# Performance work log

Hardware: AMD Instinct MI355X
Metric: run time of the kernel (lower is better)

The kernel has to match this reference:

```python
import jax, jax.numpy as jnp
import numpy as np

B, N, NPOINT, K = 16, 4096, 1024, 8
CIN, COUT = 128, 256
RADIUS = 0.2
BN_EPS = 1e-5


def fps(pts, npoint):
    # pts: [B, N, 3] -> indices [B, npoint], farthest point sampling starting at index 0
    b, n, _ = pts.shape

    def body(carry, _):
        dists, last = carry  # dists [B,N], last [B]
        cur = jnp.take_along_axis(pts, last[:, None, None], axis=1)  # [B,1,3]
        d = jnp.sum((pts - cur) ** 2, axis=-1)  # [B,N]
        dists = jnp.minimum(dists, d)
        nxt = jnp.argmax(dists, axis=-1).astype(jnp.int32)
        return (dists, nxt), last

    init = (jnp.full((b, n), jnp.finfo(pts.dtype).max, pts.dtype),
            jnp.zeros((b,), jnp.int32))
    _, idxs = jax.lax.scan(body, init, None, length=npoint)  # [npoint, B]
    return idxs.T  # [B, npoint]


def ball_query(new_xyz, pts, radius, k):
    # new_xyz [B,S,3], pts [B,N,3] -> idx [B,S,k] (pad with first in-ball index, pointnet2 semantics)
    n = pts.shape[1]
    d2 = jnp.sum((new_xyz[:, :, None, :] - pts[:, None, :, :]) ** 2, axis=-1)  # [B,S,N]
    cand = jnp.where(d2 <= radius * radius, jnp.arange(n, dtype=jnp.int32), n)
    idx = jnp.sort(cand, axis=-1)[..., :k]  # first k in-ball indices (center always in-ball)
    idx = jnp.where(idx == n, idx[..., :1], idx)
    return idx


def setup_inputs() -> dict:
    key = jax.random.key(0)
    ks = jax.random.split(key, 8)
    xyz = jax.random.uniform(ks[0], (B, 3, N), dtype=jnp.float32)
    feat = jax.random.normal(ks[1], (B, CIN, N), dtype=jnp.float32)
    conv_w = jax.random.normal(ks[2], (COUT, CIN), dtype=jnp.float32) * (1.0 / np.sqrt(CIN))
    conv_b = jax.random.normal(ks[3], (COUT,), dtype=jnp.float32) * 0.01
    bn_gamma = jax.random.uniform(ks[4], (COUT,), dtype=jnp.float32, minval=0.5, maxval=1.5)
    bn_beta = jax.random.normal(ks[5], (COUT,), dtype=jnp.float32) * 0.1
    bn_mean = jax.random.normal(ks[6], (COUT,), dtype=jnp.float32) * 0.1
    bn_var = jax.random.uniform(ks[7], (COUT,), dtype=jnp.float32, minval=0.5, maxval=1.5)
    return {"xyz": xyz, "feat": feat, "conv_w": conv_w, "conv_b": conv_b,
            "bn_gamma": bn_gamma, "bn_beta": bn_beta, "bn_mean": bn_mean, "bn_var": bn_var}


def reference(xyz, feat, conv_w, conv_b, bn_gamma, bn_beta, bn_mean, bn_var):
    pts = jnp.transpose(xyz, (0, 2, 1))   # [B,N,3]
    fts = jnp.transpose(feat, (0, 2, 1))  # [B,N,F]

    fps_idx = fps(pts, NPOINT)                                        # [B,S]
    new_xyz = jnp.take_along_axis(pts, fps_idx[..., None], axis=1)    # [B,S,3]

    idx = ball_query(new_xyz, pts, RADIUS, K)                          # [B,S,K]
    grouped = jax.vmap(lambda f, i: f[i])(fts, idx)                    # [B,S,K,F]

    # shared pointwise Conv1d (kernel 1) + BatchNorm (inference stats) + ReLU
    x = jnp.einsum('bskf,of->bsko', grouped, conv_w) + conv_b          # [B,S,K,COUT]
    x = bn_gamma * (x - bn_mean) / jnp.sqrt(bn_var + BN_EPS) + bn_beta
    x = jax.nn.relu(x)
    new_feat = jnp.max(x, axis=2)                                      # [B,S,COUT]
    return new_xyz, new_feat
```

## Files before the change

kernel.cpp:

```cpp
#include <hip/hip_runtime.h>
#include <hip/hip_bf16.h>
#include <stdint.h>

#define Bn   16
#define Nn   4096
#define Sn   1024
#define Kn   8
#define CINn 128
#define COUTn 256

static __device__ __forceinline__ float sqdist(float ax, float ay, float az,
                                               float bx, float by, float bz) {
    float dx = __fsub_rn(ax, bx);
    float dy = __fsub_rn(ay, by);
    float dz = __fsub_rn(az, bz);
    return __fadd_rn(__fadd_rn(__fmul_rn(dx, dx), __fmul_rn(dy, dy)), __fmul_rn(dz, dz));
}

static __device__ __forceinline__ unsigned long long u64max(unsigned long long a,
                                                            unsigned long long b) {
    return a > b ? a : b;
}

template <int CTRL>
static __device__ __forceinline__ void dpp_max_level(int& lo, int& hi) {
    int olo = __builtin_amdgcn_update_dpp(lo, lo, CTRL, 0xF, 0xF, false);
    int ohi = __builtin_amdgcn_update_dpp(hi, hi, CTRL, 0xF, 0xF, false);
    unsigned long long o = ((unsigned long long)(unsigned)ohi << 32) | (unsigned)olo;
    unsigned long long k = ((unsigned long long)(unsigned)hi << 32) | (unsigned)lo;
    if (o > k) { lo = olo; hi = ohi; }
}

static __device__ __forceinline__ unsigned long long wave_max_u64(unsigned long long key) {
    int lo = (int)(unsigned)(key & 0xFFFFFFFFull);
    int hi = (int)(unsigned)(key >> 32);
    dpp_max_level<0x111>(lo, hi);
    dpp_max_level<0x112>(lo, hi);
    dpp_max_level<0x114>(lo, hi);
    dpp_max_level<0x118>(lo, hi);
    dpp_max_level<0x142>(lo, hi);
    dpp_max_level<0x143>(lo, hi);
    unsigned flo = (unsigned)__builtin_amdgcn_readlane(lo, 63);
    unsigned fhi = (unsigned)__builtin_amdgcn_readlane(hi, 63);
    return ((unsigned long long)fhi << 32) | flo;
}

__global__ __launch_bounds__(256) void k_fps(const float* __restrict__ xyz,
                                             float* __restrict__ out_xyz) {
    __shared__ __align__(16) float xs[Nn], ys[Nn], zs[Nn];
    __shared__ __align__(16) unsigned long long gbuf[2][4];
    const int b = blockIdx.x;
    const int tid = threadIdx.x;
    const int wid = tid >> 6, lane = tid & 63;
    const float* base = xyz + (size_t)b * 3 * Nn;
    for (int i = tid; i < Nn; i += 256) {
        xs[i] = base[i];
        ys[i] = base[Nn + i];
        zs[i] = base[2 * Nn + i];
    }
    __syncthreads();
    float px[16], py[16], pz[16], dist[16];
#pragma unroll
    for (int j = 0; j < 16; ++j) {
        int p = tid + j * 256;
        px[j] = xs[p]; py[j] = ys[p]; pz[j] = zs[p];
        dist[j] = 3.402823466e+38f;
    }
    int last = 0;
    if (tid == 0) {
        out_xyz[(size_t)(b * Sn) * 3 + 0] = xs[0];
        out_xyz[(size_t)(b * Sn) * 3 + 1] = ys[0];
        out_xyz[(size_t)(b * Sn) * 3 + 2] = zs[0];
    }
    for (int s = 1; s < Sn; ++s) {
        const float cx = xs[last], cy = ys[last], cz = zs[last];
        float mv = -1.0f; int mi = 0;
#pragma unroll
        for (int j = 0; j < 16; ++j) {
            float d = sqdist(px[j], py[j], pz[j], cx, cy, cz);
            float nd = fminf(dist[j], d);
            dist[j] = nd;
            if (nd > mv) { mv = nd; mi = tid + j * 256; }
        }
        unsigned long long key =
            ((unsigned long long)__float_as_uint(mv) << 32) | (unsigned)(Nn - 1 - mi);
        key = wave_max_u64(key);
        if (lane == 0) gbuf[s & 1][wid] = key;
        __syncthreads();
        const ulonglong2 g0 = *(const ulonglong2*)&gbuf[s & 1][0];
        const ulonglong2 g1 = *(const ulonglong2*)&gbuf[s & 1][2];
        key = u64max(u64max(g0.x, g0.y), u64max(g1.x, g1.y));
        const int nl = Nn - 1 - (int)(unsigned)(key & 0xFFFFFFFFull);
        if (tid == 0) {
            out_xyz[(size_t)(b * Sn + s) * 3 + 0] = xs[nl];
            out_xyz[(size_t)(b * Sn + s) * 3 + 1] = ys[nl];
            out_xyz[(size_t)(b * Sn + s) * 3 + 2] = zs[nl];
        }
        last = nl;
    }
}

static __device__ __forceinline__ void wave_ball(const float* __restrict__ base,
                                                 float cx, float cy, float cz,
                                                 int lane, int* bslot) {
    int cnt = 0;
    int idx0 = -1;
    for (int chunk = 0; chunk < Nn / 64; ++chunk) {
        const int p = chunk * 64 + lane;
        const float d2 = sqdist(base[p], base[Nn + p], base[2 * Nn + p], cx, cy, cz);
        const bool in = (d2 <= 0.04f);
        const unsigned long long m = __ballot(in);
        if (m != 0ull) {
            if (idx0 < 0) idx0 = chunk * 64 + __builtin_ctzll(m);
            const int rank = cnt + __popcll(m & ((1ull << lane) - 1ull));
            if (in && rank < Kn)
                bslot[rank] = p;
            cnt += __popcll(m);
            if (cnt >= Kn) break;
        }
    }
    if (lane < Kn && lane >= cnt)
        bslot[lane] = idx0;
}

__global__ __launch_bounds__(512) void k_feat(const float* __restrict__ xyz,
                                              const float* __restrict__ out_xyz,
                                              const float* __restrict__ feat,
                                              const float* __restrict__ conv_w,
                                              const float* __restrict__ conv_b,
                                              const float* __restrict__ bn_g,
                                              const float* __restrict__ bn_b,
                                              const float* __restrict__ bn_m,
                                              const float* __restrict__ bn_v,
                                              float* __restrict__ out_feat) {
    __shared__ float Wc[32][COUTn + 1];
    __shared__ __align__(16) float At[8][Kn][36];
    __shared__ int bidx[8][Kn];
    const int tid = threadIdx.x;
    const int wave = tid >> 6, lane = tid & 63;
    const int b  = blockIdx.x & 15;
    const int c0 = (blockIdx.x >> 4) * 8;
    const int bs = b * Sn + c0 + wave;

    const float* base = xyz + (size_t)b * 3 * Nn;
    const float cx = out_xyz[(size_t)bs * 3 + 0];
    const float cy = out_xyz[(size_t)bs * 3 + 1];
    const float cz = out_xyz[(size_t)bs * 3 + 2];
    wave_ball(base, cx, cy, cz, lane, &bidx[wave][0]);

    int pt[Kn];
#pragma unroll
    for (int k = 0; k < Kn; ++k) pt[k] = bidx[wave][k];

    const float* fb = feat + (size_t)b * CINn * Nn;
    const float4* cw4 = (const float4*)conv_w;
    const int fl = lane & 31;
    const int kh = lane >> 5;
    const int wo = tid >> 3;
    const int wf = tid & 7;

    float acc[4][Kn];
#pragma unroll
    for (int j = 0; j < 4; ++j)
#pragma unroll
        for (int k = 0; k < Kn; ++k) acc[j][k] = 0.0f;

    float stgA[4];
#pragma unroll
    for (int kk = 0; kk < 4; ++kk) {
        const int ptk = kh ? pt[kk * 2 + 1] : pt[kk * 2];
        stgA[kk] = fb[(size_t)fl * Nn + ptk];
    }
    float4 stgW[4];
#pragma unroll
    for (int i = 0; i < 4; ++i) {
        const int o = wo + 64 * i;
        stgW[i] = cw4[(size_t)o * 32 + wf];
    }

#pragma unroll
    for (int fc = 0; fc < 4; ++fc) {
#pragma unroll
        for (int kk = 0; kk < 4; ++kk)
            At[wave][kk * 2 + kh][fl] = stgA[kk];
#pragma unroll
        for (int i = 0; i < 4; ++i) {
            const int o = wo + 64 * i;
            Wc[wf * 4 + 0][o] = stgW[i].x;
            Wc[wf * 4 + 1][o] = stgW[i].y;
            Wc[wf * 4 + 2][o] = stgW[i].z;
            Wc[wf * 4 + 3][o] = stgW[i].w;
        }
        __syncthreads();
        if (fc < 3) {
#pragma unroll
            for (int kk = 0; kk < 4; ++kk) {
                const int ptk = kh ? pt[kk * 2 + 1] : pt[kk * 2];
                stgA[kk] = fb[(size_t)((fc + 1) * 32 + fl) * Nn + ptk];
            }
#pragma unroll
            for (int i = 0; i < 4; ++i) {
                const int o = wo + 64 * i;
                stgW[i] = cw4[(size_t)o * 32 + (fc + 1) * 8 + wf];
            }
        }
#pragma unroll
        for (int f4l = 0; f4l < 8; ++f4l) {
            float wreg[4][4];
#pragma unroll
            for (int c = 0; c < 4; ++c) {
                const float* wrow = &Wc[f4l * 4 + c][lane];
                wreg[c][0] = wrow[0];
                wreg[c][1] = wrow[64];
                wreg[c][2] = wrow[128];
                wreg[c][3] = wrow[192];
            }
#pragma unroll
            for (int khf = 0; khf < 2; ++khf) {
                float4 fv4[4];
#pragma unroll
                for (int kk = 0; kk < 4; ++kk)
                    fv4[kk] = *(const float4*)&At[wave][khf * 4 + kk][f4l * 4];
#pragma unroll
                for (int c = 0; c < 4; ++c)
#pragma unroll
                    for (int j = 0; j < 4; ++j)
#pragma unroll
                        for (int kk = 0; kk < 4; ++kk)
                            acc[j][khf * 4 + kk] +=
                                ((const float*)&fv4[kk])[c] * wreg[c][j];
            }
        }
        __syncthreads();
    }

#pragma unroll
    for (int j = 0; j < 4; ++j) {
        const int o = lane + 64 * j;
        const float bias = conv_b[o];
        const float g = bn_g[o], be = bn_b[o], mn = bn_m[o], vr = bn_v[o];
        const float inv = sqrtf(vr + 1e-5f);
        float mx = -3.402823466e+38f;
#pragma unroll
        for (int k = 0; k < Kn; ++k) {
            float z = acc[j][k] + bias;
            float y = g * (z - mn) / inv + be;
            y = fmaxf(y, 0.0f);
            mx = fmaxf(mx, y);
        }
        out_feat[(size_t)bs * COUTn + o] = mx;
    }
}

extern "C" void kernel_launch(void* const* d_in, const int* in_sizes, int n_in,
                              void* d_out, int out_size, void* d_ws, size_t ws_size,
                              hipStream_t stream) {
    const float* xyz    = (const float*)d_in[0];
    const float* feat   = (const float*)d_in[1];
    const float* conv_w = (const float*)d_in[2];
    const float* conv_b = (const float*)d_in[3];
    const float* bn_g   = (const float*)d_in[4];
    const float* bn_b   = (const float*)d_in[5];
    const float* bn_m   = (const float*)d_in[6];
    const float* bn_v   = (const float*)d_in[7];

    float* out_xyz  = (float*)d_out;
    float* out_feat = out_xyz + (size_t)Bn * Sn * 3;

    k_fps <<<dim3(Bn),           dim3(256), 0, stream>>>(xyz, out_xyz);
    k_feat<<<dim3(Bn * Sn / 8),  dim3(512), 0, stream>>>(xyz, out_xyz, feat,
                                                         conv_w, conv_b,
                                                         bn_g, bn_b, bn_m, bn_v,
                                                         out_feat);
}
```

Before: 836.9 us.

## Use bf16 MFMA for the grouped pointwise conv in k_feat

Replaces the scalar fp32 FMA conv in k_feat with 16x16x32 bf16 MFMA instructions. Gathered features and conv weights are converted to bf16 and staged in LDS in a row layout. Each wave computes a 16-row tile of grouped points against 128 output channels, and the K-max is finished with a lane shuffle. This cuts ALU work in the GEMM part, but lowers precision to bf16 inputs and adds a full-block sync after the ball query. FPS is likely the dominant cost and is untouched.

Measured after the change: 707.3 us, median of 3. 15.5% less time.

```diff
diff --git a/kernel.cpp b/kernel.cpp
--- a/kernel.cpp
+++ b/kernel.cpp
@@ -9,6 +9,11 @@
 #define CINn 128
 #define COUTn 256
 
+typedef __attribute__((ext_vector_type(8))) short bf16x8;
+typedef __attribute__((ext_vector_type(4))) float f32x4;
+typedef unsigned short ushort;
+typedef __attribute__((ext_vector_type(8))) unsigned short ushort8;
+
 static __device__ __forceinline__ float sqdist(float ax, float ay, float az,
                                                float bx, float by, float bz) {
     float dx = __fsub_rn(ax, bx);
@@ -20,6 +25,12 @@
 static __device__ __forceinline__ unsigned long long u64max(unsigned long long a,
                                                             unsigned long long b) {
     return a > b ? a : b;
+}
+
+static __device__ __forceinline__ ushort f2bf(float f) {
+    unsigned x = __float_as_uint(f);
+    unsigned r = x + 0x7FFFu + ((x >> 16) & 1u);
+    return (ushort)(r >> 16);
 }
 
 template <int CTRL>
@@ -133,8 +144,8 @@
                                               const float* __restrict__ bn_m,
                                               const float* __restrict__ bn_v,
                                               float* __restrict__ out_feat) {
-    __shared__ float Wc[32][COUTn + 1];
-    __shared__ __align__(16) float At[8][Kn][36];
+    __shared__ __align__(16) ushort A_lds[64][136];
+    __shared__ __align__(16) ushort Wc[COUTn][40];
     __shared__ int bidx[8][Kn];
     const int tid = threadIdx.x;
     const int wave = tid >> 6, lane = tid & 63;
@@ -147,108 +158,89 @@
     const float cy = out_xyz[(size_t)bs * 3 + 1];
     const float cz = out_xyz[(size_t)bs * 3 + 2];
     wave_ball(base, cx, cy, cz, lane, &bidx[wave][0]);
-
-    int pt[Kn];
-#pragma unroll
-    for (int k = 0; k < Kn; ++k) pt[k] = bidx[wave][k];
+    __syncthreads();
 
     const float* fb = feat + (size_t)b * CINn * Nn;
-    const float4* cw4 = (const float4*)conv_w;
-    const int fl = lane & 31;
-    const int kh = lane >> 5;
-    const int wo = tid >> 3;
-    const int wf = tid & 7;
-
-    float acc[4][Kn];
-#pragma unroll
-    for (int j = 0; j < 4; ++j)
-#pragma unroll
-        for (int k = 0; k < Kn; ++k) acc[j][k] = 0.0f;
-
-    float stgA[4];
-#pragma unroll
-    for (int kk = 0; kk < 4; ++kk) {
-        const int ptk = kh ? pt[kk * 2 + 1] : pt[kk * 2];
-        stgA[kk] = fb[(size_t)fl * Nn + ptk];
-    }
+    {
+        const int r = tid >> 3, fo = tid & 7;
+        const int pt = bidx[r >> 3][r & 7];
+        ushort us[16];
+#pragma unroll
+        for (int i = 0; i < 16; ++i)
+            us[i] = f2bf(fb[(size_t)(fo * 16 + i) * Nn + pt]);
+        *(ushort8*)&A_lds[r][fo * 16]     = *(const ushort8*)&us[0];
+        *(ushort8*)&A_lds[r][fo * 16 + 8] = *(const ushort8*)&us[8];
+    }
+
+    const int wo = tid >> 1, wfh = tid & 1;
     float4 stgW[4];
-#pragma unroll
-    for (int i = 0; i < 4; ++i) {
-        const int o = wo + 64 * i;
-        stgW[i] = cw4[(size_t)o * 32 + wf];
-    }
-
-#pragma unroll
-    for (int fc = 0; fc < 4; ++fc) {
-#pragma unroll
-        for (int kk = 0; kk < 4; ++kk)
-            At[wave][kk * 2 + kh][fl] = stgA[kk];
-#pragma unroll
-        for (int i = 0; i < 4; ++i) {
-            const int o = wo + 64 * i;
-            Wc[wf * 4 + 0][o] = stgW[i].x;
-            Wc[wf * 4 + 1][o] = stgW[i].y;
-            Wc[wf * 4 + 2][o] = stgW[i].z;
-            Wc[wf * 4 + 3][o] = stgW[i].w;
+    {
+        const float4* src = (const float4*)(conv_w + (size_t)wo * CINn + wfh * 16);
+#pragma unroll
+        for (int i = 0; i < 4; ++i) stgW[i] = src[i];
+    }
+
+    const int mt = wave & 3;
+    const int obase = (wave >> 2) * 128;
+    f32x4 acc[8];
+#pragma unroll
+    for (int t = 0; t < 8; ++t) acc[t] = (f32x4){0.f, 0.f, 0.f, 0.f};
+
+    const int arow = mt * 16 + (lane & 15);
+    const int kgrp = (lane >> 4) * 8;
+
+#pragma unroll
+    for (int ks = 0; ks < 4; ++ks) {
+        {
+            ushort us[16];
+#pragma unroll
+            for (int i = 0; i < 4; ++i) {
+                us[i * 4 + 0] = f2bf(stgW[i].x);
+                us[i * 4 + 1] = f2bf(stgW[i].y);
+                us[i * 4 + 2] = f2bf(stgW[i].z);
+                us[i * 4 + 3] = f2bf(stgW[i].w);
+            }
+            *(ushort8*)&Wc[wo][wfh * 16]     = *(const ushort8*)&us[0];
+            *(ushort8*)&Wc[wo][wfh * 16 + 8] = *(const ushort8*)&us[8];
         }
         __syncthreads();
-        if (fc < 3) {
-#pragma unroll
-            for (int kk = 0; kk < 4; ++kk) {
-                const int ptk = kh ? pt[kk * 2 + 1] : pt[kk * 2];
-                stgA[kk] = fb[(size_t)((fc + 1) * 32 + fl) * Nn + ptk];
-            }
-#pragma unroll
-            for (int i = 0; i < 4; ++i) {
-                const int o = wo + 64 * i;
-                stgW[i] = cw4[(size_t)o * 32 + (fc + 1) * 8 + wf];
-            }
-        }
-#pragma unroll
-        for (int f4l = 0; f4l < 8; ++f4l) {
-            float wreg[4][4];
-#pragma unroll
-            for (int c = 0; c < 4; ++c) {
-                const float* wrow = &Wc[f4l * 4 + c][lane];
-                wreg[c][0] = wrow[0];
-                wreg[c][1] = wrow[64];
-                wreg[c][2] = wrow[128];
-                wreg[c][3] = wrow[192];
-            }
-#pragma unroll
-            for (int khf = 0; khf < 2; ++khf) {
-                float4 fv4[4];
-#pragma unroll
-                for (int kk = 0; kk < 4; ++kk)
-                    fv4[kk] = *(const float4*)&At[wave][khf * 4 + kk][f4l * 4];
-#pragma unroll
-                for (int c = 0; c < 4; ++c)
-#pragma unroll
-                    for (int j = 0; j < 4; ++j)
-#pragma unroll
-                        for (int kk = 0; kk < 4; ++kk)
-                            acc[j][khf * 4 + kk] +=
-                                ((const float*)&fv4[kk])[c] * wreg[c][j];
-            }
+        if (ks < 3) {
+            const float4* src = (const float4*)(conv_w + (size_t)wo * CINn +
+                                                (ks + 1) * 32 + wfh * 16);
+#pragma unroll
+            for (int i = 0; i < 4; ++i) stgW[i] = src[i];
+        }
+        const bf16x8 a = *(const bf16x8*)&A_lds[arow][ks * 32 + kgrp];
+#pragma unroll
+        for (int t = 0; t < 8; ++t) {
+            const int o = obase + t * 16 + (lane & 15);
+            const bf16x8 bb = *(const bf16x8*)&Wc[o][kgrp];
+            acc[t] = __builtin_amdgcn_mfma_f32_16x16x32_bf16(a, bb, acc[t], 0, 0, 0);
         }
         __syncthreads();
     }
 
-#pragma unroll
-    for (int j = 0; j < 4; ++j) {
-        const int o = lane + 64 * j;
+    const int half = lane >> 4;
+#pragma unroll
+    for (int t = 0; t < 8; ++t) {
+        const int o = obase + t * 16 + (lane & 15);
         const float bias = conv_b[o];
         const float g = bn_g[o], be = bn_b[o], mn = bn_m[o], vr = bn_v[o];
         const float inv = sqrtf(vr + 1e-5f);
-        float mx = -3.402823466e+38f;
-#pragma unroll
-        for (int k = 0; k < Kn; ++k) {
-            float z = acc[j][k] + bias;
+        float m4 = -3.402823466e+38f;
+#pragma unroll
+        for (int i = 0; i < 4; ++i) {
+            float z = acc[t][i] + bias;
             float y = g * (z - mn) / inv + be;
             y = fmaxf(y, 0.0f);
-            mx = fmaxf(mx, y);
-        }
-        out_feat[(size_t)bs * COUTn + o] = mx;
+            m4 = fmaxf(m4, y);
+        }
+        const float mo = __shfl_xor(m4, 16);
+        const float mx = fmaxf(m4, mo);
+        if (half == 0)
+            out_feat[(size_t)(b * Sn + c0 + mt * 2) * COUTn + o] = mx;
+        else if (half == 2)
+            out_feat[(size_t)(b * Sn + c0 + mt * 2 + 1) * COUTn + o] = mx;
     }
 }
 
```
